# Optimization experiments

Hardware: AMD Instinct MI355X
Metric: run time of the kernel (lower is better)

Reference implementation:

```python
import jax, jax.numpy as jnp
import numpy as np

N_NODES = 100000
N_EDGES = 1600000
IN_DIM = 512
HID_DIM = 64
N_CLASSES = 10
N_GRAPHS = 64


def setup_inputs() -> dict:
    key = jax.random.key(0)
    ks = jax.random.split(key, 8)
    x = jax.random.normal(ks[0], (N_NODES, IN_DIM), dtype=jnp.float32)
    edge_src = jax.random.randint(ks[1], (N_EDGES,), 0, N_NODES)
    edge_dst = jax.random.randint(ks[2], (N_EDGES,), 0, N_NODES)
    node2graph = jnp.sort(jax.random.randint(ks[3], (N_NODES,), 0, N_GRAPHS))
    W1 = jax.random.normal(ks[4], (IN_DIM, HID_DIM), dtype=jnp.float32) * (1.0 / np.sqrt(IN_DIM))
    b1 = jnp.zeros((HID_DIM,), dtype=jnp.float32)
    W2 = jax.random.normal(ks[5], (HID_DIM, N_CLASSES), dtype=jnp.float32) * (1.0 / np.sqrt(HID_DIM))
    b2 = jnp.zeros((N_CLASSES,), dtype=jnp.float32)
    return {"x": x, "edge_src": edge_src, "edge_dst": edge_dst,
            "node2graph": node2graph, "n_graphs": N_GRAPHS,
            "W1": W1, "b1": b1, "W2": W2, "b2": b2}


def reference(x, edge_src, edge_dst, node2graph, n_graphs, W1, b1, W2, b2):
    n = x.shape[0]
    ones_e = jnp.ones(edge_src.shape[0], dtype=x.dtype)
    # DGL GraphConv norm='both': src scaled by out-deg^-1/2, dst by in-deg^-1/2 (degrees clamped to 1)
    out_deg = jax.ops.segment_sum(ones_e, edge_src, num_segments=n)
    in_deg = jax.ops.segment_sum(ones_e, edge_dst, num_segments=n)
    src_norm = jax.lax.rsqrt(jnp.maximum(out_deg, 1.0))  # [N]
    dst_norm = jax.lax.rsqrt(jnp.maximum(in_deg, 1.0))   # [N]

    def graph_conv(h, W, b):
        h = (h * src_norm[:, None]) @ W                       # [N, out]
        agg = jax.ops.segment_sum(h[edge_src], edge_dst, num_segments=n)  # SpMM
        return agg * dst_norm[:, None] + b

    h = jax.nn.relu(graph_conv(x, W1, b1))
    h = graph_conv(h, W2, b2)
    # dgl.mean_nodes: per-graph mean over nodes
    counts = jax.ops.segment_sum(jnp.ones(n, dtype=x.dtype), node2graph, num_segments=n_graphs)
    sums = jax.ops.segment_sum(h, node2graph, num_segments=n_graphs)
    return sums / jnp.maximum(counts, 1.0)[:, None]
```

## Files before the change

kernel.cpp:

```cpp
#include <hip/hip_runtime.h>

#define NN 100000
#define NE 1600000
#define NG 64
#define BPB  50
#define NBUK 2000
#define NBUK2 2048
#define ECAP 1120
#define GPART 128
#define PREPB 128
#define ZEROB 3
#define GSTB ((NN+255)/256)

using bf16x8 = __attribute__((ext_vector_type(8))) short;
using f32x4  = __attribute__((ext_vector_type(4))) float;

__device__ inline unsigned short f2bf(float f){
    union { float f; unsigned u; } v; v.f = f;
    unsigned r = (v.u + 0x7FFFu + ((v.u >> 16) & 1u)) >> 16;
    return (unsigned short)r;
}

__global__ __launch_bounds__(256) void k_start(const int* __restrict__ src, const int* __restrict__ dst,
                                               int* __restrict__ cntD, int* __restrict__ cntS, int E,
                                               const float* __restrict__ W1, short* __restrict__ Wb,
                                               float* __restrict__ pooled,
                                               const int* __restrict__ n2g, int* __restrict__ gstart, int N){
    __shared__ int hD[NBUK2], hS[NBUK2];
    int bid = blockIdx.x;
    int tid = threadIdx.x;
    if (bid < GPART){
        for (int i=tid; i<NBUK2; i+=256){ hD[i]=0; hS[i]=0; }
        __syncthreads();
        int chunk = (E + GPART - 1)/GPART;
        int start = bid*chunk;
        int end   = min(E, start + chunk);
        for (int e = start + tid; e < end; e += 256){
            atomicAdd(&hS[src[e]/BPB], 1);
            atomicAdd(&hD[dst[e]/BPB], 1);
        }
        __syncthreads();
        for (int i=tid; i<NBUK2; i+=256){
            cntD[bid*NBUK2 + i] = hD[i];
            cntS[bid*NBUK2 + i] = hS[i];
        }
    } else if (bid < GPART+PREPB){
        int i = (bid-GPART)*256 + tid;
        if (i < 512*64){
            int k = i >> 6, c = i & 63;
            int g = k >> 5, r = k & 31, s = r >> 3, j = r & 7;
            Wb[(((g*4+s)*64 + c) << 3) + j] = (short)f2bf(W1[i]);
        }
    } else if (bid < GPART+PREPB+ZEROB){
        int i = (bid-GPART-PREPB)*256 + tid;
        if (i < NG*10) pooled[i] = 0.f;
    } else {
        int n = (bid-GPART-PREPB-ZEROB)*256 + tid;
        if (n < N){
            int g  = n2g[n];
            int gp = (n == 0) ? -1 : n2g[n-1];
            if (gp != g){
                for (int gg = gp+1; gg <= g; ++gg) gstart[gg] = n;
            }
            if (n == N-1){
                for (int gg = g+1; gg <= NG; ++gg) gstart[gg] = N;
            }
        }
    }
}

__global__ __launch_bounds__(256) void k_scanA(const int* __restrict__ cntD, const int* __restrict__ cntS,
                                               int* __restrict__ totD, int* __restrict__ totS){
    int t = blockIdx.x*256 + threadIdx.x;
    int sD=0, sS=0;
    for (int b=0;b<GPART;b++){ sD += cntD[b*NBUK2+t]; sS += cntS[b*NBUK2+t]; }
    totD[t]=sD; totS[t]=sS;
}

__global__ __launch_bounds__(1024) void k_scanB(const int* __restrict__ totD, const int* __restrict__ totS,
                                                int* __restrict__ bstartD, int* __restrict__ bstartS){
    __shared__ int sd[1024];
    int t = threadIdx.x;
    {
        int v0 = totD[2*t], v1 = totD[2*t+1];
        sd[t] = v0+v1; __syncthreads();
        for (int off=1; off<1024; off<<=1){
            int tv = (t >= off) ? sd[t-off] : 0;
            __syncthreads();
            sd[t] += tv;
            __syncthreads();
        }
        int excl = sd[t] - v0 - v1;
        if (2*t   <= NBUK) bstartD[2*t]   = excl;
        if (2*t+1 <= NBUK) bstartD[2*t+1] = excl + v0;
        __syncthreads();
    }
    {
        int v0 = totS[2*t], v1 = totS[2*t+1];
        sd[t] = v0+v1; __syncthreads();
        for (int off=1; off<1024; off<<=1){
            int tv = (t >= off) ? sd[t-off] : 0;
            __syncthreads();
            sd[t] += tv;
            __syncthreads();
        }
        int excl = sd[t] - v0 - v1;
        if (2*t   <= NBUK) bstartS[2*t]   = excl;
        if (2*t+1 <= NBUK) bstartS[2*t+1] = excl + v0;
    }
}

__global__ __launch_bounds__(256) void k_scanC(int* __restrict__ cntD, int* __restrict__ cntS,
                                               const int* __restrict__ bstartD, const int* __restrict__ bstartS){
    int t = blockIdx.x*256 + threadIdx.x;
    if (t < NBUK){
        int rD = bstartD[t], rS = bstartS[t];
        for (int b=0;b<GPART;b++){
            int idx = b*NBUK2 + t;
            int o = cntD[idx]; cntD[idx] = rD; rD += o;
            o = cntS[idx];     cntS[idx] = rS; rS += o;
        }
    }
}

__global__ __launch_bounds__(256) void k_scatter(const int* __restrict__ src, const int* __restrict__ dst,
                                                 const int* __restrict__ cntD, const int* __restrict__ cntS,
                                                 int2* __restrict__ pairs, int* __restrict__ srcl, int E){
    __shared__ unsigned oD[NBUK2], oS[NBUK2];
    for (int i=threadIdx.x; i<NBUK2; i+=256){
        oD[i] = (unsigned)cntD[blockIdx.x*NBUK2 + i];
        oS[i] = (unsigned)cntS[blockIdx.x*NBUK2 + i];
    }
    __syncthreads();
    int chunk = (E + GPART - 1)/GPART;
    int start = blockIdx.x*chunk;
    int end   = min(E, start + chunk);
    for (int e = start + threadIdx.x; e < end; e += 256){
        int s = src[e], d = dst[e];
        unsigned pD = atomicAdd(&oD[d/BPB], 1u);
        pairs[pD] = make_int2(s, d);
        unsigned pS = atomicAdd(&oS[s/BPB], 1u);
        srcl[pS] = s;
    }
}

__global__ __launch_bounds__(256) void k_outdeg(const int* __restrict__ srcl, const int* __restrict__ bstartS,
                                                float* __restrict__ sn, int N){
    __shared__ int c[BPB];
    int b = blockIdx.x;
    if (threadIdx.x < BPB) c[threadIdx.x] = 0;
    __syncthreads();
    int s0 = bstartS[b], s1 = bstartS[b+1];
    int base = b*BPB;
    for (int i = s0 + threadIdx.x; i < s1; i += 256)
        atomicAdd(&c[srcl[i] - base], 1);
    __syncthreads();
    int node = base + threadIdx.x;
    if (threadIdx.x < BPB && node < N)
        sn[node] = rsqrtf((float)max(c[threadIdx.x], 1));
}

__global__ __launch_bounds__(256) void k_gemm1(const float* __restrict__ x, const short* __restrict__ Wb,
                                               const float* __restrict__ sn, unsigned short* __restrict__ hb, int N){
    const int lane = threadIdx.x & 63;
    const int wid  = threadIdx.x >> 6;
    const int rowBase = blockIdx.x*64 + wid*16;
    const int mrow = lane & 15;
    const int s    = lane >> 4;

    int row  = rowBase + mrow;
    int rowc = (row < N) ? row : (N-1);

    const float4*  __restrict__ xv = (const float4*)x;
    const bf16x8*  __restrict__ wv = (const bf16x8*)Wb;

    f32x4 acc0 = {0.f,0.f,0.f,0.f};
    f32x4 acc1 = {0.f,0.f,0.f,0.f};
    f32x4 acc2 = {0.f,0.f,0.f,0.f};
    f32x4 acc3 = {0.f,0.f,0.f,0.f};

    const float4* xrow = xv + (size_t)rowc*128 + s*2;
    #pragma unroll 4
    for (int g=0; g<16; g++){
        float4 a0 = xrow[g*8 + 0];
        float4 a1 = xrow[g*8 + 1];
        bf16x8 af;
        af[0]=(short)f2bf(a0.x); af[1]=(short)f2bf(a0.y); af[2]=(short)f2bf(a0.z); af[3]=(short)f2bf(a0.w);
        af[4]=(short)f2bf(a1.x); af[5]=(short)f2bf(a1.y); af[6]=(short)f2bf(a1.z); af[7]=(short)f2bf(a1.w);
        int bbase = (g*4 + s)*64 + mrow;
        bf16x8 b0 = wv[bbase     ];
        bf16x8 b1 = wv[bbase + 16];
        bf16x8 b2 = wv[bbase + 32];
        bf16x8 b3 = wv[bbase + 48];
        acc0 = __builtin_amdgcn_mfma_f32_16x16x32_bf16(af, b0, acc0, 0, 0, 0);
        acc1 = __builtin_amdgcn_mfma_f32_16x16x32_bf16(af, b1, acc1, 0, 0, 0);
        acc2 = __builtin_amdgcn_mfma_f32_16x16x32_bf16(af, b2, acc2, 0, 0, 0);
        acc3 = __builtin_amdgcn_mfma_f32_16x16x32_bf16(af, b3, acc3, 0, 0, 0);
    }

    int orow = rowBase + s*4;
    #pragma unroll
    for (int q=0; q<4; q++){
        int rr = orow + q;
        if (rr < N){
            float scale = sn[rr];
            unsigned short* hp = hb + ((size_t)rr<<6) + mrow;
            hp[ 0] = f2bf(acc0[q] * scale);
            hp[16] = f2bf(acc1[q] * scale);
            hp[32] = f2bf(acc2[q] * scale);
            hp[48] = f2bf(acc3[q] * scale);
        }
    }
}

__global__ __launch_bounds__(256) void k_agg(const int2* __restrict__ pairs, const int* __restrict__ bstartD,
                                             const unsigned short* __restrict__ hb,
                                             const float* __restrict__ sn, const float* __restrict__ b1,
                                             const float* __restrict__ W2,
                                             float* __restrict__ h2, int* __restrict__ gsrc,
                                             int* __restrict__ glh, int N){
    __shared__ int lsrc[ECAP];
    __shared__ int lcnt[BPB];
    __shared__ int lstart[BPB+1];
    __shared__ unsigned lofs[BPB];
    __shared__ __align__(16) float w2t[10][64];
    __shared__ float b1s[64];
    __shared__ __align__(16) float a1s[BPB][68];
    int tid = threadIdx.x;
    if (tid < BPB) lcnt[tid] = 0;
    if (tid < 64)  b1s[tid] = b1[tid];
    for (int i=tid; i<640; i+=256){ int c = i>>6, k = i&63; w2t[c][k] = W2[k*10 + c]; }
    __syncthreads();

    int b = blockIdx.x;
    int nodeBase = b*BPB;
    int eb = bstartD[b], ee = bstartD[b+1];
    int ne = ee - eb;

    for (int i = tid; i < ne; i += 256){
        int2 pr = pairs[eb + i];
        atomicAdd(&lcnt[pr.y - nodeBase], 1);
    }
    __syncthreads();
    if (tid < 64){
        int v = (tid < BPB) ? lcnt[tid] : 0;
        int sI = v;
        for (int off=1; off<64; off<<=1){
            int t = __shfl_up(sI, off);
            if (tid >= off) sI += t;
        }
        if (tid < BPB){
            lstart[tid] = sI - v;
            lofs[tid]   = (unsigned)(sI - v);
            if (tid == BPB-1) lstart[BPB] = sI;
        }
    }
    __syncthreads();
    for (int i = tid; i < ne; i += 256){
        int2 pr = pairs[eb + i];
        unsigned pos = atomicAdd(&lofs[pr.y - nodeBase], 1u);
        lsrc[pos < ECAP ? pos : ECAP-1] = pr.x;
    }
    __syncthreads();

    for (int i = tid; i < ne; i += 256) gsrc[eb + i] = lsrc[i];
    if (tid <= BPB) glh[b*64 + tid] = eb + lstart[tid];

    int lane = tid & 63, wid = tid >> 6;
    int q  = lane >> 4;
    int c4 = lane & 15;

    for (int nl = wid; nl < BPB; nl += 4){
        int node = nodeBase + nl;
        int s0 = lstart[nl];
        int m  = lstart[nl+1] - s0;

        float a0=0.f, a1f=0.f, a2=0.f, a3=0.f;
        int j = 0;
        for (; j + 8 <= m; j += 8){
            int sa = lsrc[s0 + j + q];
            int sb = lsrc[s0 + j + 4 + q];
            uint2 va = *(const uint2*)(hb + ((size_t)sa<<6) + (c4<<2));
            uint2 vb = *(const uint2*)(hb + ((size_t)sb<<6) + (c4<<2));
            a0  += __uint_as_float((va.x & 0xffffu) << 16);
            a1f += __uint_as_float(va.x & 0xffff0000u);
            a2  += __uint_as_float((va.y & 0xffffu) << 16);
            a3  += __uint_as_float(va.y & 0xffff0000u);
            a0  += __uint_as_float((vb.x & 0xffffu) << 16);
            a1f += __uint_as_float(vb.x & 0xffff0000u);
            a2  += __uint_as_float((vb.y & 0xffffu) << 16);
            a3  += __uint_as_float(vb.y & 0xffff0000u);
        }
        for (; j < m; j += 4){
            int idx = j + q;
            int idxc = (idx < m) ? idx : (m-1);
            int sa = lsrc[s0 + idxc];
            uint2 va = *(const uint2*)(hb + ((size_t)sa<<6) + (c4<<2));
            if (idx < m){
                a0  += __uint_as_float((va.x & 0xffffu) << 16);
                a1f += __uint_as_float(va.x & 0xffff0000u);
                a2  += __uint_as_float((va.y & 0xffffu) << 16);
                a3  += __uint_as_float(va.y & 0xffff0000u);
            }
        }
        a0  += __shfl_xor(a0, 16);  a0  += __shfl_xor(a0, 32);
        a1f += __shfl_xor(a1f, 16); a1f += __shfl_xor(a1f, 32);
        a2  += __shfl_xor(a2, 16);  a2  += __shfl_xor(a2, 32);
        a3  += __shfl_xor(a3, 16);  a3  += __shfl_xor(a3, 32);

        float dnv = rsqrtf((float)max(m, 1));
        float snv = sn[node];
        float r0 = fmaxf(fmaf(a0,  dnv, b1s[(c4<<2)+0]), 0.f) * snv;
        float r1 = fmaxf(fmaf(a1f, dnv, b1s[(c4<<2)+1]), 0.f) * snv;
        float r2 = fmaxf(fmaf(a2,  dnv, b1s[(c4<<2)+2]), 0.f) * snv;
        float r3 = fmaxf(fmaf(a3,  dnv, b1s[(c4<<2)+3]), 0.f) * snv;
        if (q == 0){
            *(float4*)(&a1s[nl][c4<<2]) = make_float4(r0, r1, r2, r3);
        }
    }
    __syncthreads();

    for (int i = tid; i < BPB*10; i += 256){
        int nl = i / 10;
        int c  = i - nl*10;
        int node = nodeBase + nl;
        if (node < N){
            const float4* ap = (const float4*)(&a1s[nl][0]);
            const float4* wp = (const float4*)(&w2t[c][0]);
            float acc = 0.f;
            #pragma unroll
            for (int p=0;p<16;p++){
                float4 a = ap[p]; float4 w = wp[p];
                acc = fmaf(a.x, w.x, fmaf(a.y, w.y, fmaf(a.z, w.z, fmaf(a.w, w.w, acc))));
            }
            h2[(size_t)node*10 + c] = acc;
        }
    }
}

__global__ __launch_bounds__(256) void k_pool2(const int* __restrict__ gsrc, const int* __restrict__ glh,
                                               const float* __restrict__ h2, const int* __restrict__ n2g,
                                               float* __restrict__ pooled, int N){
    __shared__ float accS[NG*10];
    int tid = threadIdx.x;
    for (int i=tid; i<NG*10; i+=256) accS[i] = 0.f;
    __syncthreads();
    int b = blockIdx.x;
    int nodeBase = b*BPB;
    int lane = tid & 63, wid = tid >> 6;
    int e6 = lane/10, c = lane - e6*10;
    bool active = (lane < 60);

    for (int nl = wid; nl < BPB; nl += 4){
        int node = nodeBase + nl;
        int base = glh[b*64 + nl];
        int m    = glh[b*64 + nl + 1] - base;
        float acc = 0.f;
        for (int j = 0; j < m; j += 6){
            int idx = j + e6;
            int idxc = (idx < m) ? idx : (m-1);
            int srcn = gsrc[base + idxc];
            float v = h2[(size_t)srcn*10 + c];
            if (active && idx < m) acc += v;
        }
        float t0 = __shfl(acc, lane+30); if (lane < 30) acc += t0;
        float t1 = __shfl(acc, lane+10);
        float t2 = __shfl(acc, lane+20);
        if (lane < 10){
            acc += t1 + t2;
            float dnv = rsqrtf((float)max(m, 1));
            int g = n2g[node];
            atomicAdd(&accS[g*10 + lane], dnv*acc);
        }
    }
    __syncthreads();
    int g0 = n2g[nodeBase], g1 = n2g[nodeBase + BPB - 1];
    int lo = g0*10, hi = g1*10 + 10;
    for (int i = lo + tid; i < hi; i += 256)
        atomicAdd(&pooled[i], accS[i]);
}

__global__ void k_out(const float* __restrict__ pooled, const int* __restrict__ gstart,
                      const float* __restrict__ b2, float* __restrict__ out){
    int i = blockIdx.x*blockDim.x + threadIdx.x;
    if (i < NG*10){
        int g = i/10, c = i - g*10;
        float cnt = (float)max(gstart[g+1] - gstart[g], 1);
        out[i] = pooled[i]/cnt + b2[c];
    }
}

extern "C" void kernel_launch(void* const* d_in, const int* in_sizes, int n_in,
                              void* d_out, int out_size, void* d_ws, size_t ws_size,
                              hipStream_t stream) {
    const float* x    = (const float*)d_in[0];
    const int*   esrc = (const int*)d_in[1];
    const int*   edst = (const int*)d_in[2];
    const int*   n2g  = (const int*)d_in[3];
    const float* W1   = (const float*)d_in[5];
    const float* b1   = (const float*)d_in[6];
    const float* W2   = (const float*)d_in[7];
    const float* b2   = (const float*)d_in[8];
    float* out = (float*)d_out;
    const int N = in_sizes[3];
    const int E = in_sizes[1];

    char* ws = (char*)d_ws;
    size_t off = 0;
    auto alloc = [&](size_t bytes) -> void* {
        void* p = ws + off;
        off = (off + bytes + 255) & ~(size_t)255;
        return p;
    };
    float* pooled  = (float*)alloc(NG*10*4);
    int*   cntD    = (int*)alloc((size_t)GPART*NBUK2*4);
    int*   cntS    = (int*)alloc((size_t)GPART*NBUK2*4);
    int*   totD    = (int*)alloc(NBUK2*4);
    int*   totS    = (int*)alloc(NBUK2*4);
    int*   bstartD = (int*)alloc((NBUK+1)*4);
    int*   bstartS = (int*)alloc((NBUK+1)*4);
    int2*  pairs   = (int2*)alloc((size_t)E*8);
    int*   srcl    = (int*)alloc((size_t)E*4);
    int*   gsrc    = (int*)alloc((size_t)E*4);
    int*   glh     = (int*)alloc((size_t)NBUK*64*4);
    float* sn      = (float*)alloc((size_t)N*4);
    int*   gstart  = (int*)alloc((size_t)(NG+1)*4);
    short* Wb      = (short*)alloc((size_t)512*64*2);
    unsigned short* hb = (unsigned short*)alloc((size_t)N*64*2);
    float* h2      = (float*)alloc((size_t)N*10*4);

    k_start<<<dim3(GPART+PREPB+ZEROB+GSTB), dim3(256), 0, stream>>>(
        esrc, edst, cntD, cntS, E, W1, Wb, pooled, n2g, gstart, N);
    k_scanA<<<dim3(8), dim3(256), 0, stream>>>(cntD, cntS, totD, totS);
    k_scanB<<<dim3(1), dim3(1024), 0, stream>>>(totD, totS, bstartD, bstartS);
    k_scanC<<<dim3(8), dim3(256), 0, stream>>>(cntD, cntS, bstartD, bstartS);
    k_scatter<<<dim3(GPART), dim3(256), 0, stream>>>(esrc, edst, cntD, cntS, pairs, srcl, E);
    k_outdeg<<<dim3(NBUK), dim3(256), 0, stream>>>(srcl, bstartS, sn, N);

    k_gemm1<<<dim3((N+63)/64), dim3(256), 0, stream>>>(x, Wb, sn, hb, N);

    k_agg<<<dim3(NBUK), dim3(256), 0, stream>>>(pairs, bstartD, hb, sn, b1, W2, h2, gsrc, glh, N);
    k_pool2<<<dim3(NBUK), dim3(256), 0, stream>>>(gsrc, glh, h2, n2g, pooled, N);
    k_out<<<dim3(3), dim3(256), 0, stream>>>(pooled, gstart, b2, out);
}
```

Measured before the change: 244.8 us.

## Pack edge pairs into one int, double GEMM rows per wave, hardware bf16 convert

Several independent changes. Edge (src,dst) pairs become a single 32-bit word (src<<6 | local dst), which halves pair traffic in scatter and aggregation. The first GEMM handles 32 rows per wave so each W1 fragment load is reused twice, and it converts fp32 to bf16 with the packed v_cvt_pk_bf16_f32 instruction instead of manual rounding. The aggregation inner loop is unrolled to 16 gathers, and the histogram/scatter partition count is doubled. The extra partitions grow the cntD/cntS buffers and make the serial scanC loop longer, and the packed encoding relies on src < 2^25 and BPB <= 64.

```diff
diff --git a/kernel.cpp b/kernel.cpp
--- a/kernel.cpp
+++ b/kernel.cpp
@@ -7,7 +7,7 @@
 #define NBUK 2000
 #define NBUK2 2048
 #define ECAP 1120
-#define GPART 128
+#define GPART 256
 #define PREPB 128
 #define ZEROB 3
 #define GSTB ((NN+255)/256)
@@ -19,6 +19,15 @@
     union { float f; unsigned u; } v; v.f = f;
     unsigned r = (v.u + 0x7FFFu + ((v.u >> 16) & 1u)) >> 16;
     return (unsigned short)r;
+}
+
+__device__ inline bf16x8 cvt8(float4 a, float4 b){
+    union { unsigned u[4]; bf16x8 v; } r;
+    asm("v_cvt_pk_bf16_f32 %0, %1, %2" : "=v"(r.u[0]) : "v"(a.x), "v"(a.y));
+    asm("v_cvt_pk_bf16_f32 %0, %1, %2" : "=v"(r.u[1]) : "v"(a.z), "v"(a.w));
+    asm("v_cvt_pk_bf16_f32 %0, %1, %2" : "=v"(r.u[2]) : "v"(b.x), "v"(b.y));
+    asm("v_cvt_pk_bf16_f32 %0, %1, %2" : "=v"(r.u[3]) : "v"(b.z), "v"(b.w));
+    return r.v;
 }
 
 __global__ __launch_bounds__(256) void k_start(const int* __restrict__ src, const int* __restrict__ dst,
@@ -125,7 +134,7 @@
 
 __global__ __launch_bounds__(256) void k_scatter(const int* __restrict__ src, const int* __restrict__ dst,
                                                  const int* __restrict__ cntD, const int* __restrict__ cntS,
-                                                 int2* __restrict__ pairs, int* __restrict__ srcl, int E){
+                                                 int* __restrict__ pairs, int* __restrict__ srcl, int E){
     __shared__ unsigned oD[NBUK2], oS[NBUK2];
     for (int i=threadIdx.x; i<NBUK2; i+=256){
         oD[i] = (unsigned)cntD[blockIdx.x*NBUK2 + i];
@@ -137,8 +146,9 @@
     int end   = min(E, start + chunk);
     for (int e = start + threadIdx.x; e < end; e += 256){
         int s = src[e], d = dst[e];
-        unsigned pD = atomicAdd(&oD[d/BPB], 1u);
-        pairs[pD] = make_int2(s, d);
+        int bk = d/BPB;
+        unsigned pD = atomicAdd(&oD[bk], 1u);
+        pairs[pD] = (s << 6) | (d - bk*BPB);
         unsigned pS = atomicAdd(&oS[s/BPB], 1u);
         srcl[pS] = s;
     }
@@ -164,56 +174,70 @@
                                                const float* __restrict__ sn, unsigned short* __restrict__ hb, int N){
     const int lane = threadIdx.x & 63;
     const int wid  = threadIdx.x >> 6;
-    const int rowBase = blockIdx.x*64 + wid*16;
+    const int rowBase = blockIdx.x*128 + wid*32;
     const int mrow = lane & 15;
     const int s    = lane >> 4;
 
-    int row  = rowBase + mrow;
-    int rowc = (row < N) ? row : (N-1);
-
-    const float4*  __restrict__ xv = (const float4*)x;
-    const bf16x8*  __restrict__ wv = (const bf16x8*)Wb;
-
-    f32x4 acc0 = {0.f,0.f,0.f,0.f};
-    f32x4 acc1 = {0.f,0.f,0.f,0.f};
-    f32x4 acc2 = {0.f,0.f,0.f,0.f};
-    f32x4 acc3 = {0.f,0.f,0.f,0.f};
-
-    const float4* xrow = xv + (size_t)rowc*128 + s*2;
-    #pragma unroll 4
+    int rowA = rowBase + mrow;
+    int rowB = rowBase + 16 + mrow;
+    int rcA = (rowA < N) ? rowA : (N-1);
+    int rcB = (rowB < N) ? rowB : (N-1);
+
+    const float4* __restrict__ xv = (const float4*)x;
+    const bf16x8* __restrict__ wv = (const bf16x8*)Wb;
+    const float4* xrA = xv + (size_t)rcA*128 + s*2;
+    const float4* xrB = xv + (size_t)rcB*128 + s*2;
+
+    f32x4 accA0 = {0,0,0,0}, accA1 = {0,0,0,0}, accA2 = {0,0,0,0}, accA3 = {0,0,0,0};
+    f32x4 accB0 = {0,0,0,0}, accB1 = {0,0,0,0}, accB2 = {0,0,0,0}, accB3 = {0,0,0,0};
+
+    #pragma unroll 2
     for (int g=0; g<16; g++){
-        float4 a0 = xrow[g*8 + 0];
-        float4 a1 = xrow[g*8 + 1];
-        bf16x8 af;
-        af[0]=(short)f2bf(a0.x); af[1]=(short)f2bf(a0.y); af[2]=(short)f2bf(a0.z); af[3]=(short)f2bf(a0.w);
-        af[4]=(short)f2bf(a1.x); af[5]=(short)f2bf(a1.y); af[6]=(short)f2bf(a1.z); af[7]=(short)f2bf(a1.w);
+        float4 a0 = xrA[g*8 + 0];
+        float4 a1 = xrA[g*8 + 1];
+        float4 c0 = xrB[g*8 + 0];
+        float4 c1 = xrB[g*8 + 1];
+        bf16x8 afA = cvt8(a0, a1);
+        bf16x8 afB = cvt8(c0, c1);
         int bbase = (g*4 + s)*64 + mrow;
         bf16x8 b0 = wv[bbase     ];
         bf16x8 b1 = wv[bbase + 16];
         bf16x8 b2 = wv[bbase + 32];
         bf16x8 b3 = wv[bbase + 48];
-        acc0 = __builtin_amdgcn_mfma_f32_16x16x32_bf16(af, b0, acc0, 0, 0, 0);
-        acc1 = __builtin_amdgcn_mfma_f32_16x16x32_bf16(af, b1, acc1, 0, 0, 0);
-        acc2 = __builtin_amdgcn_mfma_f32_16x16x32_bf16(af, b2, acc2, 0, 0, 0);
-        acc3 = __builtin_amdgcn_mfma_f32_16x16x32_bf16(af, b3, acc3, 0, 0, 0);
-    }
-
-    int orow = rowBase + s*4;
+        accA0 = __builtin_amdgcn_mfma_f32_16x16x32_bf16(afA, b0, accA0, 0, 0, 0);
+        accA1 = __builtin_amdgcn_mfma_f32_16x16x32_bf16(afA, b1, accA1, 0, 0, 0);
+        accA2 = __builtin_amdgcn_mfma_f32_16x16x32_bf16(afA, b2, accA2, 0, 0, 0);
+        accA3 = __builtin_amdgcn_mfma_f32_16x16x32_bf16(afA, b3, accA3, 0, 0, 0);
+        accB0 = __builtin_amdgcn_mfma_f32_16x16x32_bf16(afB, b0, accB0, 0, 0, 0);
+        accB1 = __builtin_amdgcn_mfma_f32_16x16x32_bf16(afB, b1, accB1, 0, 0, 0);
+        accB2 = __builtin_amdgcn_mfma_f32_16x16x32_bf16(afB, b2, accB2, 0, 0, 0);
+        accB3 = __builtin_amdgcn_mfma_f32_16x16x32_bf16(afB, b3, accB3, 0, 0, 0);
+    }
+
     #pragma unroll
     for (int q=0; q<4; q++){
-        int rr = orow + q;
+        int rr = rowBase + s*4 + q;
         if (rr < N){
             float scale = sn[rr];
             unsigned short* hp = hb + ((size_t)rr<<6) + mrow;
-            hp[ 0] = f2bf(acc0[q] * scale);
-            hp[16] = f2bf(acc1[q] * scale);
-            hp[32] = f2bf(acc2[q] * scale);
-            hp[48] = f2bf(acc3[q] * scale);
-        }
-    }
-}
-
-__global__ __launch_bounds__(256) void k_agg(const int2* __restrict__ pairs, const int* __restrict__ bstartD,
+            hp[ 0] = f2bf(accA0[q] * scale);
+            hp[16] = f2bf(accA1[q] * scale);
+            hp[32] = f2bf(accA2[q] * scale);
+            hp[48] = f2bf(accA3[q] * scale);
+        }
+        int r2 = rowBase + 16 + s*4 + q;
+        if (r2 < N){
+            float scale = sn[r2];
+            unsigned short* hp = hb + ((size_t)r2<<6) + mrow;
+            hp[ 0] = f2bf(accB0[q] * scale);
+            hp[16] = f2bf(accB1[q] * scale);
+            hp[32] = f2bf(accB2[q] * scale);
+            hp[48] = f2bf(accB3[q] * scale);
+        }
+    }
+}
+
+__global__ __launch_bounds__(256) void k_agg(const int* __restrict__ pairs, const int* __restrict__ bstartD,
                                              const unsigned short* __restrict__ hb,
                                              const float* __restrict__ sn, const float* __restrict__ b1,
                                              const float* __restrict__ W2,
@@ -238,8 +262,8 @@
     int ne = ee - eb;
 
     for (int i = tid; i < ne; i += 256){
-        int2 pr = pairs[eb + i];
-        atomicAdd(&lcnt[pr.y - nodeBase], 1);
+        int pr = pairs[eb + i];
+        atomicAdd(&lcnt[pr & 63], 1);
     }
     __syncthreads();
     if (tid < 64){
@@ -257,9 +281,9 @@
     }
     __syncthreads();
     for (int i = tid; i < ne; i += 256){
-        int2 pr = pairs[eb + i];
-        unsigned pos = atomicAdd(&lofs[pr.y - nodeBase], 1u);
-        lsrc[pos < ECAP ? pos : ECAP-1] = pr.x;
+        int pr = pairs[eb + i];
+        unsigned pos = atomicAdd(&lofs[pr & 63], 1u);
+        lsrc[pos < ECAP ? pos : ECAP-1] = pr >> 6;
     }
     __syncthreads();
 
@@ -277,19 +301,33 @@
 
         float a0=0.f, a1f=0.f, a2=0.f, a3=0.f;
         int j = 0;
+        for (; j + 16 <= m; j += 16){
+            int sa = lsrc[s0 + j + q];
+            int sb = lsrc[s0 + j + 4 + q];
+            int sc = lsrc[s0 + j + 8 + q];
+            int sd = lsrc[s0 + j + 12 + q];
+            uint2 va = *(const uint2*)(hb + ((size_t)sa<<6) + (c4<<2));
+            uint2 vb = *(const uint2*)(hb + ((size_t)sb<<6) + (c4<<2));
+            uint2 vc = *(const uint2*)(hb + ((size_t)sc<<6) + (c4<<2));
+            uint2 vd = *(const uint2*)(hb + ((size_t)sd<<6) + (c4<<2));
+            a0  += __uint_as_float((va.x & 0xffffu) << 16) + __uint_as_float((vb.x & 0xffffu) << 16)
+                 + __uint_as_float((vc.x & 0xffffu) << 16) + __uint_as_float((vd.x & 0xffffu) << 16);
+            a1f += __uint_as_float(va.x & 0xffff0000u) + __uint_as_float(vb.x & 0xffff0000u)
+                 + __uint_as_float(vc.x & 0xffff0000u) + __uint_as_float(vd.x & 0xffff0000u);
+            a2  += __uint_as_float((va.y & 0xffffu) << 16) + __uint_as_float((vb.y & 0xffffu) << 16)
+                 + __uint_as_float((vc.y & 0xffffu) << 16) + __uint_as_float((vd.y & 0xffffu) << 16);
+            a3  += __uint_as_float(va.y & 0xffff0000u) + __uint_as_float(vb.y & 0xffff0000u)
+                 + __uint_as_float(vc.y & 0xffff0000u) + __uint_as_float(vd.y & 0xffff0000u);
+        }
         for (; j + 8 <= m; j += 8){
             int sa = lsrc[s0 + j + q];
             int sb = lsrc[s0 + j + 4 + q];
             uint2 va = *(const uint2*)(hb + ((size_t)sa<<6) + (c4<<2));
             uint2 vb = *(const uint2*)(hb + ((size_t)sb<<6) + (c4<<2));
-            a0  += __uint_as_float((va.x & 0xffffu) << 16);
-            a1f += __uint_as_float(va.x & 0xffff0000u);
-            a2  += __uint_as_float((va.y & 0xffffu) << 16);
-            a3  += __uint_as_float(va.y & 0xffff0000u);
-            a0  += __uint_as_float((vb.x & 0xffffu) << 16);
-            a1f += __uint_as_float(vb.x & 0xffff0000u);
-            a2  += __uint_as_float((vb.y & 0xffffu) << 16);
-            a3  += __uint_as_float(vb.y & 0xffff0000u);
+            a0  += __uint_as_float((va.x & 0xffffu) << 16) + __uint_as_float((vb.x & 0xffffu) << 16);
+            a1f += __uint_as_float(va.x & 0xffff0000u) + __uint_as_float(vb.x & 0xffff0000u);
+            a2  += __uint_as_float((va.y & 0xffffu) << 16) + __uint_as_float((vb.y & 0xffffu) << 16);
+            a3  += __uint_as_float(va.y & 0xffff0000u) + __uint_as_float(vb.y & 0xffff0000u);
         }
         for (; j < m; j += 4){
             int idx = j + q;
@@ -419,7 +457,7 @@
     int*   totS    = (int*)alloc(NBUK2*4);
     int*   bstartD = (int*)alloc((NBUK+1)*4);
     int*   bstartS = (int*)alloc((NBUK+1)*4);
-    int2*  pairs   = (int2*)alloc((size_t)E*8);
+    int*   pairs   = (int*)alloc((size_t)E*4);
     int*   srcl    = (int*)alloc((size_t)E*4);
     int*   gsrc    = (int*)alloc((size_t)E*4);
     int*   glh     = (int*)alloc((size_t)NBUK*64*4);
@@ -437,7 +475,7 @@
     k_scatter<<<dim3(GPART), dim3(256), 0, stream>>>(esrc, edst, cntD, cntS, pairs, srcl, E);
     k_outdeg<<<dim3(NBUK), dim3(256), 0, stream>>>(srcl, bstartS, sn, N);
 
-    k_gemm1<<<dim3((N+63)/64), dim3(256), 0, stream>>>(x, Wb, sn, hb, N);
+    k_gemm1<<<dim3((N+127)/128), dim3(256), 0, stream>>>(x, Wb, sn, hb, N);
 
     k_agg<<<dim3(NBUK), dim3(256), 0, stream>>>(pairs, bstartD, hb, sn, b1, W2, h2, gsrc, glh, N);
     k_pool2<<<dim3(NBUK), dim3(256), 0, stream>>>(gsrc, glh, h2, n2g, pooled, N);
```

Result: no change. 241.4 us (-1.4%).
